# Kernel tuning notes

Measured on AMD Instinct MI355X. Metric: run time of the kernel, lower is better.

The kernel has to match this reference:

```python
import math
import jax, jax.numpy as jnp
import numpy as np

NUM_HEADS = 12


def _key_blocks(x, w):
    # x: [B,S,H,D] -> overlapping key blocks [B, C, 3w, H, D], block c covers
    # original key positions [c*w - w, c*w + 2w) (zero padded at the edges).
    B, S, H, D = x.shape
    C = S // w
    x_pad = jnp.pad(x, ((0, 0), (w, w), (0, 0), (0, 0)))
    idx = (jnp.arange(C) * w)[:, None] + jnp.arange(3 * w)[None, :]  # [C,3w]
    return x_pad[:, idx]


def _band_qk(q, k, w):
    # banded_gemm_qk: scores[b,i,h,j] = q[b,i,h,:] . k[b,i+j-w,h,:], j in [0,2w]
    B, S, H, D = q.shape
    C = S // w
    kb = _key_blocks(k, w)                       # [B,C,3w,H,D]
    qb = q.reshape(B, C, w, H, D)
    s = jnp.einsum('bcxhd,bcyhd->bchxy', qb, kb)  # [B,C,H,w,3w]
    row = jnp.arange(w)[:, None]
    col = row + jnp.arange(2 * w + 1)[None, :]    # diagonal extraction
    band = s[:, :, :, row, col]                   # [B,C,H,w,2w+1]
    return band.transpose(0, 1, 3, 2, 4).reshape(B, S, H, 2 * w + 1)


def _band_pv(p, v, w):
    # banded_gemm_pv: out[b,i,h,:] = sum_j p[b,i,h,j] * v[b,i+j-w,h,:]
    B, S, H, M = p.shape
    C = S // w
    vb = _key_blocks(v, w)                        # [B,C,3w,H,D]
    pb = p.reshape(B, C, w, H, M).transpose(0, 1, 3, 2, 4)  # [B,C,H,w,2w+1]
    row = jnp.arange(w)[:, None]
    col = row + jnp.arange(2 * w + 1)[None, :]
    p_full = jnp.zeros((B, C, H, w, 3 * w), p.dtype).at[:, :, :, row, col].set(pb)
    out = jnp.einsum('bchxy,bcyhd->bcxhd', p_full, vb)  # [B,C,w,H,D]
    return out.reshape(B, S, H, -1)


def setup_inputs():
    key = jax.random.key(0)
    ks = jax.random.split(key, 14)
    B, S, E, G = 2, 4096, 768, 64
    scale = 0.02
    hs = jax.random.normal(ks[0], (B, S, E), jnp.float32)
    mask = jnp.zeros((B, 1, 1, S), jnp.int32).at[:, :, :, :G].set(1)
    def lin(k):
        kw, kb = jax.random.split(k)
        return (jax.random.normal(kw, (E, E), jnp.float32) * scale,
                jax.random.normal(kb, (E,), jnp.float32) * scale)
    Wq, bq = lin(ks[1]); Wk, bk = lin(ks[2]); Wv, bv = lin(ks[3])
    Wqg, bqg = lin(ks[4]); Wkg, bkg = lin(ks[5]); Wvg, bvg = lin(ks[6])
    return dict(hidden_states=hs, attention_mask=mask,
                Wq=Wq, bq=bq, Wk=Wk, bk=bk, Wv=Wv, bv=bv,
                Wqg=Wqg, bqg=bqg, Wkg=Wkg, bkg=bkg, Wvg=Wvg, bvg=bvg,
                window=256, num_global=G)


def reference(hidden_states, attention_mask, Wq, bq, Wk, bk, Wv, bv,
              Wqg, bqg, Wkg, bkg, Wvg, bvg, window, num_global):
    B, S, E = hidden_states.shape
    H = NUM_HEADS
    D = E // H
    w, G = window, num_global
    inv_sqrt_d = 1.0 / math.sqrt(D)

    mask2d = attention_mask.reshape(B, S)
    removed = mask2d != 0  # global (or padding) keys excluded from windowed attn

    q = (hidden_states @ Wq + bq) * inv_sqrt_d
    k = hidden_states @ Wk + bk
    v = hidden_states @ Wv + bv
    q = q.reshape(B, S, H, D)
    k = k.reshape(B, S, H, D)
    v = v.reshape(B, S, H, D)

    # --- local (banded) attention scores ---
    band = _band_qk(q, k, w)                                  # [B,S,H,2w+1]
    key_pos = jnp.arange(S)[:, None] + jnp.arange(-w, w + 1)[None, :]  # [S,2w+1]
    valid = (key_pos >= 0) & (key_pos < S)
    removed_pad = jnp.pad(removed, ((0, 0), (w, w)))
    band_removed = removed_pad[:, key_pos + w]                # [B,S,2w+1]
    keep = valid[None, :, None, :] & (~band_removed)[:, :, None, :]
    band = jnp.where(keep, band, -jnp.inf)

    # --- every-token -> global-token scores (global tokens are first G) ---
    sel = jnp.einsum('blhd,bshd->blhs', q, k[:, :G])          # [B,S,H,G]
    scores = jnp.concatenate([sel, band], axis=-1)            # [B,S,H,G+2w+1]
    probs = jax.nn.softmax(scores.astype(jnp.float32), axis=-1)

    out = jnp.einsum('blhs,bshd->blhd', probs[..., :G], v[:, :G].astype(jnp.float32))
    out = out + _band_pv(probs[..., G:], v.astype(jnp.float32), w)
    out = out.astype(hidden_states.dtype).reshape(B, S, E)

    # --- global tokens attend to everything (separate projections) ---
    hg = hidden_states[:, :G]
    qg = (hg @ Wqg + bqg).reshape(B, G, H, D)
    kg = (hidden_states @ Wkg + bkg).reshape(B, S, H, D)
    vg = (hidden_states @ Wvg + bvg).reshape(B, S, H, D)
    gs = jnp.einsum('bghd,bshd->bhgs', qg, kg) * inv_sqrt_d   # [B,H,G,S]
    gp = jax.nn.softmax(gs.astype(jnp.float32), axis=-1)
    go = jnp.einsum('bhgs,bshd->bghd', gp, vg.astype(jnp.float32)).reshape(B, G, E)
    out = out.at[:, :G].set(go.astype(out.dtype))
    return out
```

## Files before the change

kernel.cpp:

```cpp
#include <hip/hip_runtime.h>
#include <hip/hip_bf16.h>


#define BB 2
#define SS 4096
#define EE 768
#define HH 12
#define DD 64
#define WW 256
#define GG 64
#define NSPLIT 16

typedef unsigned short u16;
typedef __attribute__((ext_vector_type(4))) float f4v;
typedef __attribute__((ext_vector_type(8))) short s8v;
typedef __attribute__((ext_vector_type(4))) short s4v;
typedef __attribute__((ext_vector_type(4))) int i4v;
typedef __attribute__((ext_vector_type(4))) unsigned short us4v;

#define MFMA_BF16(a, b, c) __builtin_amdgcn_mfma_f32_16x16x32_bf16((a), (b), (c), 0, 0, 0)

#if __has_builtin(__builtin_amdgcn_mfma_f32_16x16x16bf16_1k)
#define HAVE_MFMA16 1
#define MFMA16(a, b, c) __builtin_amdgcn_mfma_f32_16x16x16bf16_1k((a), (b), (c), 0, 0, 0)
#else
#define HAVE_MFMA16 0
#endif

constexpr long NSE     = (long)BB * SS * EE;
constexpr long OFF_HSB = 0;
constexpr long OFF_WT  = OFF_HSB + NSE;
constexpr long OFF_Q   = OFF_WT + 6L * EE * EE;
constexpr long OFF_K   = OFF_Q + NSE;
constexpr long OFF_V   = OFF_K + NSE;
constexpr long OFF_KG  = OFF_V + NSE;
constexpr long OFF_VG  = OFF_KG + NSE;
constexpr long OFF_QG  = OFF_VG + NSE;
constexpr long OFF_VT  = OFF_QG + (long)BB * GG * EE;
constexpr long OFF_VGT = OFF_VT + NSE;

constexpr long NQTILE = (long)BB * HH * 4;
constexpr int  NLB    = BB * HH * 63;

__device__ __forceinline__ u16 f2bf(float f) {
  unsigned u = __float_as_uint(f);
  u += 0x7fffu + ((u >> 16) & 1u);
  return (u16)(u >> 16);
}

__device__ __forceinline__ unsigned pk_bf16(float a, float b) {
  union { __hip_bfloat162 h; unsigned u; } c;
  c.h = __float22bfloat162_rn(make_float2(a, b));
  return c.u;
}

__global__ __launch_bounds__(256) void k_prep(const float* __restrict__ hs,
                                              const float* __restrict__ Wq, const float* __restrict__ Wk,
                                              const float* __restrict__ Wv, const float* __restrict__ Wkg,
                                              const float* __restrict__ Wvg, const float* __restrict__ Wqg,
                                              u16* __restrict__ ws) {
  int bid = blockIdx.x;
  if (bid < 6144) {
    long i = ((long)bid * 256 + threadIdx.x) * 4;
    f4v v = *(const f4v*)(hs + i);
    us4v o;
#pragma unroll
    for (int j = 0; j < 4; ++j) o[j] = f2bf(v[j]);
    *(us4v*)(ws + OFF_HSB + i) = o;
    return;
  }
  int wb = bid - 6144;
  int widx = wb / 576; int rem = wb % 576; int kt = rem / 24; int nt = rem % 24;
  const float* src;
  switch (widx) {
    case 0: src = Wq; break; case 1: src = Wk; break; case 2: src = Wv; break;
    case 3: src = Wkg; break; case 4: src = Wvg; break; default: src = Wqg; break;
  }
  __shared__ float tl[32][33];
  int t = threadIdx.x; int r = t >> 3; int c4 = (t & 7) * 4;
  f4v v = *(const f4v*)(src + (long)(kt * 32 + r) * EE + nt * 32 + c4);
#pragma unroll
  for (int j = 0; j < 4; ++j) tl[r][c4 + j] = v[j];
  __syncthreads();
  us4v o;
#pragma unroll
  for (int j = 0; j < 4; ++j) o[j] = f2bf(tl[c4 + j][r]);
  *(us4v*)(ws + OFF_WT + (long)widx * EE * EE + (long)(nt * 32 + r) * EE + kt * 32 + c4) = o;
}

__global__ __launch_bounds__(256, 4) void k_proj(u16* __restrict__ ws,
                                              const float* __restrict__ bq, const float* __restrict__ bk,
                                              const float* __restrict__ bv, const float* __restrict__ bkg,
                                              const float* __restrict__ bvg, const float* __restrict__ bqg) {
  int bid = blockIdx.x;
  int widx, mt, nt;
  if (bid < 1920) {
    int L = (bid & 7) * 240 + (bid >> 3);
    mt = L / 30; int inner = L % 30; widx = inner / 6; nt = inner % 6;
  } else { widx = 5; mt = 0; nt = bid - 1920; }

  __shared__ u16 Al[128 * 64];
  __shared__ u16 Bl[128 * 64];
  int tid = threadIdx.x, lane = tid & 63, wid = tid >> 6;
  int wr = wid >> 1, wc = wid & 1;

  f4v acc[4][4];
#pragma unroll
  for (int i = 0; i < 4; ++i)
#pragma unroll
    for (int j = 0; j < 4; ++j) acc[i][j] = f4v{0.f, 0.f, 0.f, 0.f};

  const u16* hsb = ws + OFF_HSB;
  const u16* Wp  = ws + OFF_WT + (long)widx * EE * EE;

  const u16* asrc[4]; const u16* bsrc[4];
  int dso[4];
#pragma unroll
  for (int it = 0; it < 4; ++it) {
    int c = tid + it * 256;
    int r = c >> 3, j = c & 7;
    long arow;
    if (widx == 5) { int rr = mt * 128 + r; arow = (long)(rr >> 6) * SS + (rr & 63); }
    else           { arow = (long)mt * 128 + r; }
    asrc[it] = hsb + arow * EE + j * 8;
    bsrc[it] = Wp + (long)(nt * 128 + r) * EE + j * 8;
    dso[it]  = r * 64 + (j ^ (r & 7)) * 8;
  }

  const u16* afp[4]; const u16* bfp[4];
#pragma unroll
  for (int f = 0; f < 4; ++f) {
    afp[f] = Al + (wr * 64 + f * 16 + (lane & 15)) * 64;
    bfp[f] = Bl + (wc * 64 + f * 16 + (lane & 15)) * 64;
  }
  int hi4 = lane >> 4, lx = lane & 7;

  i4v areg[4], breg[4];
#pragma unroll
  for (int it = 0; it < 4; ++it) {
    areg[it] = *(const i4v*)(asrc[it]);
    breg[it] = *(const i4v*)(bsrc[it]);
  }
#pragma unroll
  for (int it = 0; it < 4; ++it) {
    *(i4v*)&Al[dso[it]] = areg[it];
    *(i4v*)&Bl[dso[it]] = breg[it];
  }
  __syncthreads();

  for (int t = 0; t < 12; ++t) {
    if (t < 11) {
      int k0n = (t + 1) * 64;
#pragma unroll
      for (int it = 0; it < 4; ++it) {
        areg[it] = *(const i4v*)(asrc[it] + k0n);
        breg[it] = *(const i4v*)(bsrc[it] + k0n);
      }
    }
#pragma unroll
    for (int ks = 0; ks < 2; ++ks) {
      int sw = ((ks * 4 + hi4) ^ lx) * 8;
      s8v af[4], bfr[4];
#pragma unroll
      for (int f = 0; f < 4; ++f) {
        af[f]  = *(const s8v*)(afp[f] + sw);
        bfr[f] = *(const s8v*)(bfp[f] + sw);
      }
#pragma unroll
      for (int i = 0; i < 4; ++i)
#pragma unroll
        for (int j = 0; j < 4; ++j) acc[i][j] = MFMA_BF16(af[i], bfr[j], acc[i][j]);
    }
    __syncthreads();
    if (t < 11) {
#pragma unroll
      for (int it = 0; it < 4; ++it) {
        *(i4v*)&Al[dso[it]] = areg[it];
        *(i4v*)&Bl[dso[it]] = breg[it];
      }
    }
    __syncthreads();
  }

  const float* bias; u16* outp; float scl = 1.0f;
  switch (widx) {
    case 0: bias = bq;  outp = ws + OFF_Q;  scl = 0.125f * 1.44269504f; break;
    case 1: bias = bk;  outp = ws + OFF_K;  break;
    case 2: bias = bv;  outp = ws + OFF_VT;  break;
    case 3: bias = bkg; outp = ws + OFF_KG; break;
    case 4: bias = bvg; outp = ws + OFF_VGT; break;
    default: bias = bqg; outp = ws + OFF_QG; scl = 0.125f * 1.44269504f; break;
  }

  if (widx == 2 || widx == 4) {
    int s0g = mt * 128 + wr * 64 + (lane >> 4) * 4;
#pragma unroll
    for (int fi = 0; fi < 4; ++fi) {
      int srow = s0g + fi * 16;
      int b_ = srow >> 12; int sl = srow & (SS - 1);
#pragma unroll
      for (int fj = 0; fj < 4; ++fj) {
        int col = nt * 128 + wc * 64 + fj * 16 + (lane & 15);
        float bcol = bias[col];
        us4v o;
#pragma unroll
        for (int e = 0; e < 4; ++e) o[e] = f2bf(acc[fi][fj][e] + bcol);
        *(us4v*)&outp[((long)(b_ * HH + (col >> 6)) * DD + (col & 63)) * SS + sl] = o;
      }
    }
  } else {
#pragma unroll
    for (int fi = 0; fi < 4; ++fi)
#pragma unroll
      for (int fj = 0; fj < 4; ++fj) {
        int col = nt * 128 + wc * 64 + fj * 16 + (lane & 15);
        float bcol = bias[col];
#pragma unroll
        for (int e = 0; e < 4; ++e) {
          int rl = wr * 64 + fi * 16 + (lane >> 4) * 4 + e;
          float vv = (acc[fi][fj][e] + bcol) * scl;
          outp[(long)(mt * 128 + rl) * EE + col] = f2bf(vv);
        }
      }
  }
}

__global__ __launch_bounds__(256) void k_lattn(const u16* __restrict__ ws, float* __restrict__ out) {
  int bid0 = blockIdx.x;
  if (bid0 >= NLB) {
    int g = bid0 - NLB;
    int b = g / (HH * 4); int rem = g % (HH * 4); int h = rem >> 2; int qs = rem & 3;
    int tid = threadIdx.x;
    int row = tid >> 4; int c4 = (tid & 15) * 4;

    const float* PA = (const float*)(ws + OFF_V);
    const float* Pm = PA + NQTILE * NSPLIT * 1024L;
    const float* Pl2 = Pm + NQTILE * NSPLIT * 16L;
    long base = (long)g * NSPLIT;

    float M = -1e30f;
#pragma unroll
    for (int s = 0; s < NSPLIT; ++s) M = fmaxf(M, Pm[(base + s) * 16 + row]);
    f4v acc = f4v{0.f, 0.f, 0.f, 0.f};
    float L = 0.f;
#pragma unroll
    for (int s = 0; s < NSPLIT; ++s) {
      float wgt = exp2f(Pm[(base + s) * 16 + row] - M);
      L += wgt * Pl2[(base + s) * 16 + row];
      f4v a = *(const f4v*)&PA[(base + s) * 1024 + row * 64 + c4];
#pragma unroll
      for (int j = 0; j < 4; ++j) acc[j] += wgt * a[j];
    }
    float inv = 1.f / L;
    f4v o;
#pragma unroll
    for (int j = 0; j < 4; ++j) o[j] = acc[j] * inv;
    *(f4v*)&out[((long)b * SS + qs * 16 + row) * EE + h * DD + c4] = o;
    return;
  }

  int bid = (bid0 & 7) * 189 + (bid0 >> 3);
  int b = bid / (HH * 63); int rem = bid % (HH * 63); int h = rem / 63; int qt = rem % 63;
  int l0 = GG + qt * 64;
  int tid = threadIdx.x, lane = tid & 63, wid = tid >> 6;
  int l15 = lane & 15, hi4 = lane >> 4;

  __shared__ u16 Kl[64][72];
  __shared__ u16 Vtl[64][72];
#if !HAVE_MFMA16
  __shared__ u16 Pl[4][16][72];
#endif

  const u16* Qp  = ws + OFF_Q + (long)b * SS * EE;
  const u16* Kp  = ws + OFF_K + (long)b * SS * EE;
  const u16* Vtp = ws + OFF_VT + (long)(b * HH + h) * DD * SS;

  int qbase = l0 + wid * 16;
  s8v qf[2];
#pragma unroll
  for (int ks = 0; ks < 2; ++ks)
    qf[ks] = *(const s8v*)(Qp + (long)(qbase + l15) * EE + h * DD + ks * 32 + hi4 * 8);

  f4v ao[4];
#pragma unroll
  for (int df = 0; df < 4; ++df) ao[df] = f4v{0.f, 0.f, 0.f, 0.f};

  int lo = (l0 - WW > GG) ? (l0 - WW) : GG;
  int hi = (l0 + 64 + WW < SS) ? (l0 + 64 + WW) : SS;
  int ntile = 1 + ((hi - lo) >> 6);

  const u16* kbase[2]; const u16* vbase[2];
  u16* kdst[2]; u16* vdst[2];
#pragma unroll
  for (int it = 0; it < 2; ++it) {
    int c = tid + it * 256;
    int sr = c >> 3, so = (c & 7) * 8;
    kbase[it] = Kp + (long)sr * EE + h * DD + so;
    vbase[it] = Vtp + (long)sr * SS + so;
    kdst[it] = &Kl[sr][so];
    vdst[it] = &Vtl[sr][so];
  }

  i4v kreg[2], vreg[2];
#pragma unroll
  for (int it = 0; it < 2; ++it) {
    kreg[it] = *(const i4v*)(kbase[it]);
    vreg[it] = *(const i4v*)(vbase[it]);
  }
#pragma unroll
  for (int it = 0; it < 2; ++it) {
    *(i4v*)kdst[it] = kreg[it];
    *(i4v*)vdst[it] = vreg[it];
  }
  __syncthreads();

#if HAVE_MFMA16
  float m_s = -1e30f, l_p = 0.f;

  for (int t = 0; t < ntile; ++t) {
    int kb = (t == 0) ? 0 : lo + (t - 1) * 64;
    if (t + 1 < ntile) {
      int kbn = lo + t * 64;
#pragma unroll
      for (int it = 0; it < 2; ++it) {
        kreg[it] = *(const i4v*)(kbase[it] + (long)kbn * EE);
        vreg[it] = *(const i4v*)(vbase[it] + kbn);
      }
    }

    f4v sc[4];
#pragma unroll
    for (int c = 0; c < 4; ++c) sc[c] = f4v{0.f, 0.f, 0.f, 0.f};
    __builtin_amdgcn_s_setprio(1);
#pragma unroll
    for (int c = 0; c < 4; ++c)
#pragma unroll
      for (int ks = 0; ks < 2; ++ks) {
        s8v kf = *(const s8v*)&Kl[c * 16 + l15][ks * 32 + hi4 * 8];
        sc[c] = MFMA_BF16(kf, qf[ks], sc[c]);
      }
    __builtin_amdgcn_s_setprio(0);

    if (t > 0 && (kb <= l0 - WW || kb >= l0 + WW)) {
      int qrow = qbase + l15;
#pragma unroll
      for (int c = 0; c < 4; ++c)
#pragma unroll
        for (int e = 0; e < 4; ++e) {
          int key = kb + c * 16 + hi4 * 4 + e;
          if (key < qrow - WW || key > qrow + WW) sc[c][e] = -1e30f;
        }
    }

    float pmax = sc[0][0];
#pragma unroll
    for (int c = 0; c < 4; ++c)
#pragma unroll
      for (int e = 0; e < 4; ++e) pmax = fmaxf(pmax, sc[c][e]);

    bool need = (t == 0) || !__all(pmax <= m_s + 11.5f);
    if (need) {
      float rm = pmax;
      rm = fmaxf(rm, __shfl_xor(rm, 16));
      rm = fmaxf(rm, __shfl_xor(rm, 32));
      float mn = fmaxf(m_s, rm);
      float scl = exp2f(m_s - mn);
      l_p *= scl;
      float s0 = __shfl(scl, hi4 * 4 + 0);
      float s1 = __shfl(scl, hi4 * 4 + 1);
      float s2 = __shfl(scl, hi4 * 4 + 2);
      float s3 = __shfl(scl, hi4 * 4 + 3);
#pragma unroll
      for (int df = 0; df < 4; ++df) {
        ao[df][0] *= s0; ao[df][1] *= s1; ao[df][2] *= s2; ao[df][3] *= s3;
      }
      m_s = mn;
    }

    unsigned u01[4], u23[4];
#pragma unroll
    for (int c = 0; c < 4; ++c) {
      float p0 = exp2f(sc[c][0] - m_s);
      float p1 = exp2f(sc[c][1] - m_s);
      float p2 = exp2f(sc[c][2] - m_s);
      float p3 = exp2f(sc[c][3] - m_s);
      l_p += (p0 + p1) + (p2 + p3);
      u01[c] = pk_bf16(p0, p1);
      u23[c] = pk_bf16(p2, p3);
    }

    __builtin_amdgcn_s_setprio(1);
#pragma unroll
    for (int c = 0; c < 4; ++c) {
      union { s4v v; unsigned u[2]; } pa;
      pa.u[0] = u01[c]; pa.u[1] = u23[c];
#pragma unroll
      for (int df = 0; df < 4; ++df) {
        s4v vf = *(const s4v*)&Vtl[df * 16 + l15][c * 16 + hi4 * 4];
        ao[df] = MFMA16(pa.v, vf, ao[df]);
      }
    }
    __builtin_amdgcn_s_setprio(0);
    __syncthreads();

    if (t + 1 < ntile) {
#pragma unroll
      for (int it = 0; it < 2; ++it) {
        *(i4v*)kdst[it] = kreg[it];
        *(i4v*)vdst[it] = vreg[it];
      }
    }
    __syncthreads();
  }

  float l_row = l_p;
  l_row += __shfl_xor(l_row, 16);
  l_row += __shfl_xor(l_row, 32);
  float lq[4];
#pragma unroll
  for (int e = 0; e < 4; ++e) lq[e] = __shfl(l_row, hi4 * 4 + e);
#pragma unroll
  for (int df = 0; df < 4; ++df)
#pragma unroll
    for (int e = 0; e < 4; ++e) {
      int row = qbase + hi4 * 4 + e;
      int col = h * DD + df * 16 + l15;
      out[((long)b * SS + row) * EE + col] = ao[df][e] / lq[e];
    }

#else
  float m_r[4], l_p4[4];
#pragma unroll
  for (int e = 0; e < 4; ++e) { m_r[e] = -1e30f; l_p4[e] = 0.f; }

  for (int t = 0; t < ntile; ++t) {
    int kb = (t == 0) ? 0 : lo + (t - 1) * 64;
    if (t + 1 < ntile) {
      int kbn = lo + t * 64;
#pragma unroll
      for (int it = 0; it < 2; ++it) {
        kreg[it] = *(const i4v*)(kbase[it] + (long)kbn * EE);
        vreg[it] = *(const i4v*)(vbase[it] + kbn);
      }
    }

    f4v sc[4];
#pragma unroll
    for (int c = 0; c < 4; ++c) sc[c] = f4v{0.f, 0.f, 0.f, 0.f};
    __builtin_amdgcn_s_setprio(1);
#pragma unroll
    for (int c = 0; c < 4; ++c)
#pragma unroll
      for (int ks = 0; ks < 2; ++ks) {
        s8v kf = *(const s8v*)&Kl[c * 16 + l15][ks * 32 + hi4 * 8];
        sc[c] = MFMA_BF16(qf[ks], kf, sc[c]);
      }
    __builtin_amdgcn_s_setprio(0);

    if (t > 0 && (kb <= l0 - WW || kb >= l0 + WW)) {
#pragma unroll
      for (int c = 0; c < 4; ++c) {
        int key = kb + c * 16 + l15;
#pragma unroll
        for (int e = 0; e < 4; ++e) {
          int qrow = qbase + hi4 * 4 + e;
          if (key < qrow - WW || key > qrow + WW) sc[c][e] = -1e30f;
        }
      }
    }

    float pmax[4];
#pragma unroll
    for (int e = 0; e < 4; ++e)
      pmax[e] = fmaxf(fmaxf(sc[0][e], sc[1][e]), fmaxf(sc[2][e], sc[3][e]));
    bool need;
    if (t == 0) need = true;
    else {
      bool ok = (pmax[0] <= m_r[0] + 11.5f) & (pmax[1] <= m_r[1] + 11.5f) &
                (pmax[2] <= m_r[2] + 11.5f) & (pmax[3] <= m_r[3] + 11.5f);
      need = !__all(ok);
    }
    if (need) {
#pragma unroll
      for (int e = 0; e < 4; ++e) {
        float rm = pmax[e];
#pragma unroll
        for (int off = 1; off < 16; off <<= 1) rm = fmaxf(rm, __shfl_xor(rm, off));
        float mn = fmaxf(m_r[e], rm);
        float scl = exp2f(m_r[e] - mn);
        l_p4[e] *= scl;
#pragma unroll
        for (int df = 0; df < 4; ++df) ao[df][e] *= scl;
        m_r[e] = mn;
      }
    }

#pragma unroll
    for (int e = 0; e < 4; ++e) {
      float p0 = exp2f(sc[0][e] - m_r[e]);
      float p1 = exp2f(sc[1][e] - m_r[e]);
      float p2 = exp2f(sc[2][e] - m_r[e]);
      float p3 = exp2f(sc[3][e] - m_r[e]);
      l_p4[e] += (p0 + p1) + (p2 + p3);
      unsigned u01 = pk_bf16(p0, p1);
      unsigned u23 = pk_bf16(p2, p3);
      int pr = hi4 * 4 + e;
      Pl[wid][pr][l15]      = (u16)u01;
      Pl[wid][pr][16 + l15] = (u16)(u01 >> 16);
      Pl[wid][pr][32 + l15] = (u16)u23;
      Pl[wid][pr][48 + l15] = (u16)(u23 >> 16);
    }

    __builtin_amdgcn_s_setprio(1);
#pragma unroll
    for (int kblk = 0; kblk < 2; ++kblk) {
      s8v pf = *(const s8v*)&Pl[wid][l15][kblk * 32 + hi4 * 8];
#pragma unroll
      for (int df = 0; df < 4; ++df) {
        s8v vf = *(const s8v*)&Vtl[df * 16 + l15][kblk * 32 + hi4 * 8];
        ao[df] = MFMA_BF16(pf, vf, ao[df]);
      }
    }
    __builtin_amdgcn_s_setprio(0);
    __syncthreads();

    if (t + 1 < ntile) {
#pragma unroll
      for (int it = 0; it < 2; ++it) {
        *(i4v*)kdst[it] = kreg[it];
        *(i4v*)vdst[it] = vreg[it];
      }
    }
    __syncthreads();
  }

  float l_r[4];
#pragma unroll
  for (int e = 0; e < 4; ++e) {
    float s = l_p4[e];
#pragma unroll
    for (int off = 1; off < 16; off <<= 1) s += __shfl_xor(s, off);
    l_r[e] = s;
  }
#pragma unroll
  for (int df = 0; df < 4; ++df)
#pragma unroll
    for (int e = 0; e < 4; ++e) {
      int row = qbase + hi4 * 4 + e;
      int col = h * DD + df * 16 + l15;
      out[((long)b * SS + row) * EE + col] = ao[df][e] / l_r[e];
    }
#endif
}

__global__ __launch_bounds__(64) void k_gattn_part(u16* __restrict__ ws) {
  int bid = blockIdx.x;
  int g = bid / NSPLIT; int sp = bid % NSPLIT;
  int b = g / (HH * 4); int rem = g % (HH * 4); int h = rem >> 2; int qs = rem & 3;
  int lane = threadIdx.x;

  __shared__ u16 Kl[32][72];
  __shared__ u16 Vtl[64][40];
  __shared__ u16 Pl[16][40];

  const u16* Qgp = ws + OFF_QG + (long)b * GG * EE;
  const u16* Kgp = ws + OFF_KG + (long)b * SS * EE;
  const u16* Vtp = ws + OFF_VGT + (long)(b * HH + h) * DD * SS;

  int qbase = qs * 16;
  s8v qf[2];
#pragma unroll
  for (int ks = 0; ks < 2; ++ks)
    qf[ks] = *(const s8v*)(Qgp + (long)(qbase + (lane & 15)) * EE + h * DD + ks * 32 + (lane >> 4) * 8);

  float m_r[4], l_p[4]; f4v ao[4];
#pragma unroll
  for (int e = 0; e < 4; ++e) { m_r[e] = -1e30f; l_p[e] = 0.f; }
#pragma unroll
  for (int df = 0; df < 4; ++df) ao[df] = f4v{0.f, 0.f, 0.f, 0.f};

  int t0 = sp * (SS / 32 / NSPLIT);
  for (int kt = t0; kt < t0 + SS / 32 / NSPLIT; ++kt) {
    int kb = kt * 32;
#pragma unroll
    for (int r2 = 0; r2 < 4; ++r2) {
      int chunk = lane + r2 * 64;
      int kr = chunk >> 3, ko = (chunk & 7) * 8;
      *(i4v*)&Kl[kr][ko] = *(const i4v*)(Kgp + (long)(kb + kr) * EE + h * DD + ko);
      int dr = chunk >> 2, ko2 = (chunk & 3) * 8;
      *(i4v*)&Vtl[dr][ko2] = *(const i4v*)(Vtp + (long)dr * SS + kb + ko2);
    }
    __syncthreads();

    f4v sc[2] = {f4v{0.f, 0.f, 0.f, 0.f}, f4v{0.f, 0.f, 0.f, 0.f}};
#pragma unroll
    for (int c = 0; c < 2; ++c)
#pragma unroll
      for (int ks = 0; ks < 2; ++ks) {
        s8v kf = *(const s8v*)&Kl[c * 16 + (lane & 15)][ks * 32 + (lane >> 4) * 8];
        sc[c] = MFMA_BF16(qf[ks], kf, sc[c]);
      }

    float pmax[4];
#pragma unroll
    for (int e = 0; e < 4; ++e) pmax[e] = fmaxf(sc[0][e], sc[1][e]);
    bool need;
    if (kt == t0) need = true;
    else {
      bool ok = (pmax[0] <= m_r[0] + 11.5f) & (pmax[1] <= m_r[1] + 11.5f) &
                (pmax[2] <= m_r[2] + 11.5f) & (pmax[3] <= m_r[3] + 11.5f);
      need = !__all(ok);
    }
    if (need) {
#pragma unroll
      for (int e = 0; e < 4; ++e) {
        float rm = pmax[e];
#pragma unroll
        for (int off = 1; off < 16; off <<= 1) rm = fmaxf(rm, __shfl_xor(rm, off));
        float mn = fmaxf(m_r[e], rm);
        float scl = exp2f(m_r[e] - mn);
        l_p[e] *= scl;
#pragma unroll
        for (int df = 0; df < 4; ++df) ao[df][e] *= scl;
        m_r[e] = mn;
      }
    }

#pragma unroll
    for (int e = 0; e < 4; ++e) {
      float p0 = exp2f(sc[0][e] - m_r[e]);
      float p1 = exp2f(sc[1][e] - m_r[e]);
      l_p[e] += p0 + p1;
      unsigned u01 = pk_bf16(p0, p1);
      int pr = (lane >> 4) * 4 + e;
      int l15 = lane & 15;
      Pl[pr][l15]      = (u16)u01;
      Pl[pr][16 + l15] = (u16)(u01 >> 16);
    }
    s8v pf = *(const s8v*)&Pl[lane & 15][(lane >> 4) * 8];
#pragma unroll
    for (int df = 0; df < 4; ++df) {
      s8v vf = *(const s8v*)&Vtl[df * 16 + (lane & 15)][(lane >> 4) * 8];
      ao[df] = MFMA_BF16(pf, vf, ao[df]);
    }
    __syncthreads();
  }

  float l_r[4];
#pragma unroll
  for (int e = 0; e < 4; ++e) {
    float s = l_p[e];
#pragma unroll
    for (int off = 1; off < 16; off <<= 1) s += __shfl_xor(s, off);
    l_r[e] = s;
  }

  float* PA = (float*)(ws + OFF_V);
  float* Pm = PA + NQTILE * NSPLIT * 1024L;
  float* Pl2 = Pm + NQTILE * NSPLIT * 16L;
  long pb = (long)g * NSPLIT + sp;
#pragma unroll
  for (int df = 0; df < 4; ++df)
#pragma unroll
    for (int e = 0; e < 4; ++e) {
      int rl = (lane >> 4) * 4 + e;
      PA[pb * 1024 + rl * 64 + df * 16 + (lane & 15)] = ao[df][e];
    }
  if ((lane & 15) == 0) {
#pragma unroll
    for (int e = 0; e < 4; ++e) {
      int rl = (lane >> 4) * 4 + e;
      Pm[pb * 16 + rl] = m_r[e];
      Pl2[pb * 16 + rl] = l_r[e];
    }
  }
}

extern "C" void kernel_launch(void* const* d_in, const int* in_sizes, int n_in,
                              void* d_out, int out_size, void* d_ws, size_t ws_size,
                              hipStream_t stream) {
  const float* hs  = (const float*)d_in[0];
  const float* Wq  = (const float*)d_in[2];  const float* bq  = (const float*)d_in[3];
  const float* Wk  = (const float*)d_in[4];  const float* bk  = (const float*)d_in[5];
  const float* Wv  = (const float*)d_in[6];  const float* bv  = (const float*)d_in[7];
  const float* Wqg = (const float*)d_in[8];  const float* bqg = (const float*)d_in[9];
  const float* Wkg = (const float*)d_in[10]; const float* bkg = (const float*)d_in[11];
  const float* Wvg = (const float*)d_in[12]; const float* bvg = (const float*)d_in[13];
  u16* ws = (u16*)d_ws;
  float* out = (float*)d_out;

  k_prep<<<6144 + 6 * 24 * 24, 256, 0, stream>>>(hs, Wq, Wk, Wv, Wkg, Wvg, Wqg, ws);
  k_proj<<<1926, 256, 0, stream>>>(ws, bq, bk, bv, bkg, bvg, bqg);
  k_gattn_part<<<(int)(NQTILE * NSPLIT), 64, 0, stream>>>(ws);
  k_lattn<<<NLB + (int)NQTILE, 256, 0, stream>>>(ws, out);
}
```

Baseline: 134.1 us.

## Deepen projection GEMM prefetch and double-buffer attention K/V tiles

```diff
diff --git a/kernel.cpp b/kernel.cpp
--- a/kernel.cpp
+++ b/kernel.cpp
@@ -135,28 +135,19 @@
   }
   int hi4 = lane >> 4, lx = lane & 7;
 
-  i4v areg[4], breg[4];
-#pragma unroll
-  for (int it = 0; it < 4; ++it) {
-    areg[it] = *(const i4v*)(asrc[it]);
-    breg[it] = *(const i4v*)(bsrc[it]);
-  }
-#pragma unroll
-  for (int it = 0; it < 4; ++it) {
-    *(i4v*)&Al[dso[it]] = areg[it];
-    *(i4v*)&Bl[dso[it]] = breg[it];
-  }
+  i4v a0[4], b0[4], a1[4], b1[4];
+#pragma unroll
+  for (int it = 0; it < 4; ++it) { a0[it] = *(const i4v*)(asrc[it]); b0[it] = *(const i4v*)(bsrc[it]); }
+#pragma unroll
+  for (int it = 0; it < 4; ++it) { *(i4v*)&Al[dso[it]] = a0[it]; *(i4v*)&Bl[dso[it]] = b0[it]; }
+#pragma unroll
+  for (int it = 0; it < 4; ++it) { a0[it] = *(const i4v*)(asrc[it] + 64);  b0[it] = *(const i4v*)(bsrc[it] + 64); }
+#pragma unroll
+  for (int it = 0; it < 4; ++it) { a1[it] = *(const i4v*)(asrc[it] + 128); b1[it] = *(const i4v*)(bsrc[it] + 128); }
   __syncthreads();
 
+#pragma unroll
   for (int t = 0; t < 12; ++t) {
-    if (t < 11) {
-      int k0n = (t + 1) * 64;
-#pragma unroll
-      for (int it = 0; it < 4; ++it) {
-        areg[it] = *(const i4v*)(asrc[it] + k0n);
-        breg[it] = *(const i4v*)(bsrc[it] + k0n);
-      }
-    }
 #pragma unroll
     for (int ks = 0; ks < 2; ++ks) {
       int sw = ((ks * 4 + hi4) ^ lx) * 8;
@@ -173,10 +164,22 @@
     }
     __syncthreads();
     if (t < 11) {
-#pragma unroll
-      for (int it = 0; it < 4; ++it) {
-        *(i4v*)&Al[dso[it]] = areg[it];
-        *(i4v*)&Bl[dso[it]] = breg[it];
+      if ((t & 1) == 0) {
+#pragma unroll
+        for (int it = 0; it < 4; ++it) { *(i4v*)&Al[dso[it]] = a0[it]; *(i4v*)&Bl[dso[it]] = b0[it]; }
+        if (t < 9) {
+          int k0n = (t + 3) * 64;
+#pragma unroll
+          for (int it = 0; it < 4; ++it) { a0[it] = *(const i4v*)(asrc[it] + k0n); b0[it] = *(const i4v*)(bsrc[it] + k0n); }
+        }
+      } else {
+#pragma unroll
+        for (int it = 0; it < 4; ++it) { *(i4v*)&Al[dso[it]] = a1[it]; *(i4v*)&Bl[dso[it]] = b1[it]; }
+        if (t < 9) {
+          int k0n = (t + 3) * 64;
+#pragma unroll
+          for (int it = 0; it < 4; ++it) { a1[it] = *(const i4v*)(asrc[it] + k0n); b1[it] = *(const i4v*)(bsrc[it] + k0n); }
+        }
       }
     }
     __syncthreads();
@@ -265,8 +268,8 @@
   int tid = threadIdx.x, lane = tid & 63, wid = tid >> 6;
   int l15 = lane & 15, hi4 = lane >> 4;
 
-  __shared__ u16 Kl[64][72];
-  __shared__ u16 Vtl[64][72];
+  __shared__ u16 Kl[2][64][72];
+  __shared__ u16 Vtl[2][64][72];
 #if !HAVE_MFMA16
   __shared__ u16 Pl[4][16][72];
 #endif
@@ -290,15 +293,18 @@
   int ntile = 1 + ((hi - lo) >> 6);
 
   const u16* kbase[2]; const u16* vbase[2];
-  u16* kdst[2]; u16* vdst[2];
+  u16* kdstb[2][2]; u16* vdstb[2][2];
 #pragma unroll
   for (int it = 0; it < 2; ++it) {
     int c = tid + it * 256;
     int sr = c >> 3, so = (c & 7) * 8;
     kbase[it] = Kp + (long)sr * EE + h * DD + so;
     vbase[it] = Vtp + (long)sr * SS + so;
-    kdst[it] = &Kl[sr][so];
-    vdst[it] = &Vtl[sr][so];
+#pragma unroll
+    for (int bf = 0; bf < 2; ++bf) {
+      kdstb[bf][it] = &Kl[bf][sr][so];
+      vdstb[bf][it] = &Vtl[bf][sr][so];
+    }
   }
 
   i4v kreg[2], vreg[2];
@@ -309,8 +315,8 @@
   }
 #pragma unroll
   for (int it = 0; it < 2; ++it) {
-    *(i4v*)kdst[it] = kreg[it];
-    *(i4v*)vdst[it] = vreg[it];
+    *(i4v*)kdstb[0][it] = kreg[it];
+    *(i4v*)vdstb[0][it] = vreg[it];
   }
   __syncthreads();
 
@@ -318,6 +324,7 @@
   float m_s = -1e30f, l_p = 0.f;
 
   for (int t = 0; t < ntile; ++t) {
+    int cur = t & 1;
     int kb = (t == 0) ? 0 : lo + (t - 1) * 64;
     if (t + 1 < ntile) {
       int kbn = lo + t * 64;
@@ -336,7 +343,7 @@
     for (int c = 0; c < 4; ++c)
 #pragma unroll
       for (int ks = 0; ks < 2; ++ks) {
-        s8v kf = *(const s8v*)&Kl[c * 16 + l15][ks * 32 + hi4 * 8];
+        s8v kf = *(const s8v*)&Kl[cur][c * 16 + l15][ks * 32 + hi4 * 8];
         sc[c] = MFMA_BF16(kf, qf[ks], sc[c]);
       }
     __builtin_amdgcn_s_setprio(0);
@@ -396,18 +403,17 @@
       pa.u[0] = u01[c]; pa.u[1] = u23[c];
 #pragma unroll
       for (int df = 0; df < 4; ++df) {
-        s4v vf = *(const s4v*)&Vtl[df * 16 + l15][c * 16 + hi4 * 4];
+        s4v vf = *(const s4v*)&Vtl[cur][df * 16 + l15][c * 16 + hi4 * 4];
         ao[df] = MFMA16(pa.v, vf, ao[df]);
       }
     }
     __builtin_amdgcn_s_setprio(0);
-    __syncthreads();
 
     if (t + 1 < ntile) {
 #pragma unroll
       for (int it = 0; it < 2; ++it) {
-        *(i4v*)kdst[it] = kreg[it];
-        *(i4v*)vdst[it] = vreg[it];
+        *(i4v*)kdstb[cur ^ 1][it] = kreg[it];
+        *(i4v*)vdstb[cur ^ 1][it] = vreg[it];
       }
     }
     __syncthreads();
@@ -434,6 +440,7 @@
   for (int e = 0; e < 4; ++e) { m_r[e] = -1e30f; l_p4[e] = 0.f; }
 
   for (int t = 0; t < ntile; ++t) {
+    int cur = t & 1;
     int kb = (t == 0) ? 0 : lo + (t - 1) * 64;
     if (t + 1 < ntile) {
       int kbn = lo + t * 64;
@@ -452,7 +459,7 @@
     for (int c = 0; c < 4; ++c)
 #pragma unroll
       for (int ks = 0; ks < 2; ++ks) {
-        s8v kf = *(const s8v*)&Kl[c * 16 + l15][ks * 32 + hi4 * 8];
+        s8v kf = *(const s8v*)&Kl[cur][c * 16 + l15][ks * 32 + hi4 * 8];
         sc[c] = MFMA_BF16(qf[ks], kf, sc[c]);
       }
     __builtin_amdgcn_s_setprio(0);
@@ -517,18 +524,17 @@
       s8v pf = *(const s8v*)&Pl[wid][l15][kblk * 32 + hi4 * 8];
 #pragma unroll
       for (int df = 0; df < 4; ++df) {
-        s8v vf = *(const s8v*)&Vtl[df * 16 + l15][kblk * 32 + hi4 * 8];
+        s8v vf = *(const s8v*)&Vtl[cur][df * 16 + l15][kblk * 32 + hi4 * 8];
         ao[df] = MFMA_BF16(pf, vf, ao[df]);
       }
     }
     __builtin_amdgcn_s_setprio(0);
-    __syncthreads();
 
     if (t + 1 < ntile) {
 #pragma unroll
       for (int it = 0; it < 2; ++it) {
-        *(i4v*)kdst[it] = kreg[it];
-        *(i4v*)vdst[it] = vreg[it];
+        *(i4v*)kdstb[cur ^ 1][it] = kreg[it];
+        *(i4v*)vdstb[cur ^ 1][it] = vreg[it];
       }
     }
     __syncthreads();
```

Result: slower. 287.8 us (+114.6%).

## Fuse global-attention partials into local-attention launch, split combine into own kernel

Applied to the files above, without the earlier changes.

```diff
diff --git a/kernel.cpp b/kernel.cpp
--- a/kernel.cpp
+++ b/kernel.cpp
@@ -41,6 +41,7 @@
 
 constexpr long NQTILE = (long)BB * HH * 4;
 constexpr int  NLB    = BB * HH * 63;
+constexpr int  NPB    = (int)(NQTILE * NSPLIT / 4);
 
 __device__ __forceinline__ u16 f2bf(float f) {
   unsigned u = __float_as_uint(f);
@@ -225,50 +226,143 @@
   }
 }
 
-__global__ __launch_bounds__(256) void k_lattn(const u16* __restrict__ ws, float* __restrict__ out) {
+__global__ __launch_bounds__(256) void k_fused(const u16* __restrict__ ws, float* __restrict__ out) {
+  int tid = threadIdx.x, lane = tid & 63, wid = tid >> 6;
+  int l15 = lane & 15, hi4 = lane >> 4;
+  __shared__ __align__(16) char smem[44032];
   int bid0 = blockIdx.x;
+
   if (bid0 >= NLB) {
-    int g = bid0 - NLB;
+    int task = (bid0 - NLB) * 4 + wid;
+    int g = task >> 4; int sp = task & 15;
     int b = g / (HH * 4); int rem = g % (HH * 4); int h = rem >> 2; int qs = rem & 3;
-    int tid = threadIdx.x;
-    int row = tid >> 4; int c4 = (tid & 15) * 4;
-
-    const float* PA = (const float*)(ws + OFF_V);
-    const float* Pm = PA + NQTILE * NSPLIT * 1024L;
-    const float* Pl2 = Pm + NQTILE * NSPLIT * 16L;
-    long base = (long)g * NSPLIT;
-
-    float M = -1e30f;
-#pragma unroll
-    for (int s = 0; s < NSPLIT; ++s) M = fmaxf(M, Pm[(base + s) * 16 + row]);
-    f4v acc = f4v{0.f, 0.f, 0.f, 0.f};
-    float L = 0.f;
-#pragma unroll
-    for (int s = 0; s < NSPLIT; ++s) {
-      float wgt = exp2f(Pm[(base + s) * 16 + row] - M);
-      L += wgt * Pl2[(base + s) * 16 + row];
-      f4v a = *(const f4v*)&PA[(base + s) * 1024 + row * 64 + c4];
-#pragma unroll
-      for (int j = 0; j < 4; ++j) acc[j] += wgt * a[j];
-    }
-    float inv = 1.f / L;
-    f4v o;
-#pragma unroll
-    for (int j = 0; j < 4; ++j) o[j] = acc[j] * inv;
-    *(f4v*)&out[((long)b * SS + qs * 16 + row) * EE + h * DD + c4] = o;
+
+    char* base = smem + wid * 11008;
+    u16 (*Kl2)[72] = (u16(*)[72])base;
+    u16 (*Vt2)[40] = (u16(*)[40])(base + 4608);
+    u16 (*Pw)[40]  = (u16(*)[40])(base + 9728);
+
+    const u16* Qgp = ws + OFF_QG + (long)b * GG * EE;
+    const u16* Kgp = ws + OFF_KG + (long)b * SS * EE;
+    const u16* Vtp = ws + OFF_VGT + (long)(b * HH + h) * DD * SS;
+
+    int qbase = qs * 16;
+    s8v qf[2];
+#pragma unroll
+    for (int ks = 0; ks < 2; ++ks)
+      qf[ks] = *(const s8v*)(Qgp + (long)(qbase + l15) * EE + h * DD + ks * 32 + hi4 * 8);
+
+    float m_r[4], l_p[4]; f4v ao[4];
+#pragma unroll
+    for (int e = 0; e < 4; ++e) { m_r[e] = -1e30f; l_p[e] = 0.f; }
+#pragma unroll
+    for (int df = 0; df < 4; ++df) ao[df] = f4v{0.f, 0.f, 0.f, 0.f};
+
+    int t0 = sp * (SS / 32 / NSPLIT);
+    for (int kt = t0; kt < t0 + SS / 32 / NSPLIT; ++kt) {
+      int kb = kt * 32;
+#pragma unroll
+      for (int r2 = 0; r2 < 4; ++r2) {
+        int chunk = lane + r2 * 64;
+        int kr = chunk >> 3, ko = (chunk & 7) * 8;
+        *(i4v*)&Kl2[kr][ko] = *(const i4v*)(Kgp + (long)(kb + kr) * EE + h * DD + ko);
+        int dr = chunk >> 2, ko2 = (chunk & 3) * 8;
+        *(i4v*)&Vt2[dr][ko2] = *(const i4v*)(Vtp + (long)dr * SS + kb + ko2);
+      }
+      __syncthreads();
+
+      f4v sc[2] = {f4v{0.f, 0.f, 0.f, 0.f}, f4v{0.f, 0.f, 0.f, 0.f}};
+#pragma unroll
+      for (int c = 0; c < 2; ++c)
+#pragma unroll
+        for (int ks = 0; ks < 2; ++ks) {
+          s8v kf = *(const s8v*)&Kl2[c * 16 + l15][ks * 32 + hi4 * 8];
+          sc[c] = MFMA_BF16(qf[ks], kf, sc[c]);
+        }
+
+      float pmax[4];
+#pragma unroll
+      for (int e = 0; e < 4; ++e) pmax[e] = fmaxf(sc[0][e], sc[1][e]);
+      bool need;
+      if (kt == t0) need = true;
+      else {
+        bool ok = (pmax[0] <= m_r[0] + 11.5f) & (pmax[1] <= m_r[1] + 11.5f) &
+                  (pmax[2] <= m_r[2] + 11.5f) & (pmax[3] <= m_r[3] + 11.5f);
+        need = !__all(ok);
+      }
+      if (need) {
+#pragma unroll
+        for (int e = 0; e < 4; ++e) {
+          float rm = pmax[e];
+#pragma unroll
+          for (int off = 1; off < 16; off <<= 1) rm = fmaxf(rm, __shfl_xor(rm, off));
+          float mn = fmaxf(m_r[e], rm);
+          float scl = exp2f(m_r[e] - mn);
+          l_p[e] *= scl;
+#pragma unroll
+          for (int df = 0; df < 4; ++df) ao[df][e] *= scl;
+          m_r[e] = mn;
+        }
+      }
+
+#pragma unroll
+      for (int e = 0; e < 4; ++e) {
+        float p0 = exp2f(sc[0][e] - m_r[e]);
+        float p1 = exp2f(sc[1][e] - m_r[e]);
+        l_p[e] += p0 + p1;
+        unsigned u01 = pk_bf16(p0, p1);
+        int pr = hi4 * 4 + e;
+        Pw[pr][l15]      = (u16)u01;
+        Pw[pr][16 + l15] = (u16)(u01 >> 16);
+      }
+      s8v pf = *(const s8v*)&Pw[l15][hi4 * 8];
+#pragma unroll
+      for (int df = 0; df < 4; ++df) {
+        s8v vf = *(const s8v*)&Vt2[df * 16 + l15][hi4 * 8];
+        ao[df] = MFMA_BF16(pf, vf, ao[df]);
+      }
+      __syncthreads();
+    }
+
+    float l_r[4];
+#pragma unroll
+    for (int e = 0; e < 4; ++e) {
+      float s = l_p[e];
+#pragma unroll
+      for (int off = 1; off < 16; off <<= 1) s += __shfl_xor(s, off);
+      l_r[e] = s;
+    }
+
+    float* PA = (float*)(ws + OFF_V);
+    float* Pm = PA + NQTILE * NSPLIT * 1024L;
+    float* Pl2 = Pm + NQTILE * NSPLIT * 16L;
+    long pb = (long)g * NSPLIT + sp;
+#pragma unroll
+    for (int df = 0; df < 4; ++df)
+#pragma unroll
+      for (int e = 0; e < 4; ++e) {
+        int rl = hi4 * 4 + e;
+        PA[pb * 1024 + rl * 64 + df * 16 + l15] = ao[df][e];
+      }
+    if (l15 == 0) {
+#pragma unroll
+      for (int e = 0; e < 4; ++e) {
+        int rl = hi4 * 4 + e;
+        Pm[pb * 16 + rl] = m_r[e];
+        Pl2[pb * 16 + rl] = l_r[e];
+      }
+    }
     return;
   }
 
   int bid = (bid0 & 7) * 189 + (bid0 >> 3);
   int b = bid / (HH * 63); int rem = bid % (HH * 63); int h = rem / 63; int qt = rem % 63;
   int l0 = GG + qt * 64;
-  int tid = threadIdx.x, lane = tid & 63, wid = tid >> 6;
-  int l15 = lane & 15, hi4 = lane >> 4;
-
-  __shared__ u16 Kl[64][72];
-  __shared__ u16 Vtl[64][72];
+
+  u16 (*Kl)[72]  = (u16(*)[72])smem;
+  u16 (*Vtl)[72] = (u16(*)[72])(smem + 9216);
 #if !HAVE_MFMA16
-  __shared__ u16 Pl[4][16][72];
+  u16 (*Pl)[16][72] = (u16(*)[16][72])(smem + 18432);
 #endif
 
   const u16* Qp  = ws + OFF_Q + (long)b * SS * EE;
@@ -553,127 +647,35 @@
 #endif
 }
 
-__global__ __launch_bounds__(64) void k_gattn_part(u16* __restrict__ ws) {
-  int bid = blockIdx.x;
-  int g = bid / NSPLIT; int sp = bid % NSPLIT;
+__global__ __launch_bounds__(256) void k_gcomb(const u16* __restrict__ ws, float* __restrict__ out) {
+  int g = blockIdx.x;
   int b = g / (HH * 4); int rem = g % (HH * 4); int h = rem >> 2; int qs = rem & 3;
-  int lane = threadIdx.x;
-
-  __shared__ u16 Kl[32][72];
-  __shared__ u16 Vtl[64][40];
-  __shared__ u16 Pl[16][40];
-
-  const u16* Qgp = ws + OFF_QG + (long)b * GG * EE;
-  const u16* Kgp = ws + OFF_KG + (long)b * SS * EE;
-  const u16* Vtp = ws + OFF_VGT + (long)(b * HH + h) * DD * SS;
-
-  int qbase = qs * 16;
-  s8v qf[2];
-#pragma unroll
-  for (int ks = 0; ks < 2; ++ks)
-    qf[ks] = *(const s8v*)(Qgp + (long)(qbase + (lane & 15)) * EE + h * DD + ks * 32 + (lane >> 4) * 8);
-
-  float m_r[4], l_p[4]; f4v ao[4];
-#pragma unroll
-  for (int e = 0; e < 4; ++e) { m_r[e] = -1e30f; l_p[e] = 0.f; }
-#pragma unroll
-  for (int df = 0; df < 4; ++df) ao[df] = f4v{0.f, 0.f, 0.f, 0.f};
-
-  int t0 = sp * (SS / 32 / NSPLIT);
-  for (int kt = t0; kt < t0 + SS / 32 / NSPLIT; ++kt) {
-    int kb = kt * 32;
-#pragma unroll
-    for (int r2 = 0; r2 < 4; ++r2) {
-      int chunk = lane + r2 * 64;
-      int kr = chunk >> 3, ko = (chunk & 7) * 8;
-      *(i4v*)&Kl[kr][ko] = *(const i4v*)(Kgp + (long)(kb + kr) * EE + h * DD + ko);
-      int dr = chunk >> 2, ko2 = (chunk & 3) * 8;
-      *(i4v*)&Vtl[dr][ko2] = *(const i4v*)(Vtp + (long)dr * SS + kb + ko2);
-    }
-    __syncthreads();
-
-    f4v sc[2] = {f4v{0.f, 0.f, 0.f, 0.f}, f4v{0.f, 0.f, 0.f, 0.f}};
-#pragma unroll
-    for (int c = 0; c < 2; ++c)
-#pragma unroll
-      for (int ks = 0; ks < 2; ++ks) {
-        s8v kf = *(const s8v*)&Kl[c * 16 + (lane & 15)][ks * 32 + (lane >> 4) * 8];
-        sc[c] = MFMA_BF16(qf[ks], kf, sc[c]);
-      }
-
-    float pmax[4];
-#pragma unroll
-    for (int e = 0; e < 4; ++e) pmax[e] = fmaxf(sc[0][e], sc[1][e]);
-    bool need;
-    if (kt == t0) need = true;
-    else {
-      bool ok = (pmax[0] <= m_r[0] + 11.5f) & (pmax[1] <= m_r[1] + 11.5f) &
-                (pmax[2] <= m_r[2] + 11.5f) & (pmax[3] <= m_r[3] + 11.5f);
-      need = !__all(ok);
-    }
-    if (need) {
-#pragma unroll
-      for (int e = 0; e < 4; ++e) {
-        float rm = pmax[e];
-#pragma unroll
-        for (int off = 1; off < 16; off <<= 1) rm = fmaxf(rm, __shfl_xor(rm, off));
-        float mn = fmaxf(m_r[e], rm);
-        float scl = exp2f(m_r[e] - mn);
-        l_p[e] *= scl;
-#pragma unroll
-        for (int df = 0; df < 4; ++df) ao[df][e] *= scl;
-        m_r[e] = mn;
-      }
-    }
-
-#pragma unroll
-    for (int e = 0; e < 4; ++e) {
-      float p0 = exp2f(sc[0][e] - m_r[e]);
-      float p1 = exp2f(sc[1][e] - m_r[e]);
-      l_p[e] += p0 + p1;
-      unsigned u01 = pk_bf16(p0, p1);
-      int pr = (lane >> 4) * 4 + e;
-      int l15 = lane & 15;
-      Pl[pr][l15]      = (u16)u01;
-      Pl[pr][16 + l15] = (u16)(u01 >> 16);
-    }
-    s8v pf = *(const s8v*)&Pl[lane & 15][(lane >> 4) * 8];
-#pragma unroll
-    for (int df = 0; df < 4; ++df) {
-      s8v vf = *(const s8v*)&Vtl[df * 16 + (lane & 15)][(lane >> 4) * 8];
-      ao[df] = MFMA_BF16(pf, vf, ao[df]);
-    }
-    __syncthreads();
-  }
-
-  float l_r[4];
-#pragma unroll
-  for (int e = 0; e < 4; ++e) {
-    float s = l_p[e];
-#pragma unroll
-    for (int off = 1; off < 16; off <<= 1) s += __shfl_xor(s, off);
-    l_r[e] = s;
-  }
-
-  float* PA = (float*)(ws + OFF_V);
-  float* Pm = PA + NQTILE * NSPLIT * 1024L;
-  float* Pl2 = Pm + NQTILE * NSPLIT * 16L;
-  long pb = (long)g * NSPLIT + sp;
-#pragma unroll
-  for (int df = 0; df < 4; ++df)
-#pragma unroll
-    for (int e = 0; e < 4; ++e) {
-      int rl = (lane >> 4) * 4 + e;
-      PA[pb * 1024 + rl * 64 + df * 16 + (lane & 15)] = ao[df][e];
-    }
-  if ((lane & 15) == 0) {
-#pragma unroll
-    for (int e = 0; e < 4; ++e) {
-      int rl = (lane >> 4) * 4 + e;
-      Pm[pb * 16 + rl] = m_r[e];
-      Pl2[pb * 16 + rl] = l_r[e];
-    }
-  }
+  int tid = threadIdx.x;
+  int row = tid >> 4; int c4 = (tid & 15) * 4;
+
+  const float* PA = (const float*)(ws + OFF_V);
+  const float* Pm = PA + NQTILE * NSPLIT * 1024L;
+  const float* Pl2 = Pm + NQTILE * NSPLIT * 16L;
+  long base = (long)g * NSPLIT;
+
+  float M = -1e30f;
+#pragma unroll
+  for (int s = 0; s < NSPLIT; ++s) M = fmaxf(M, Pm[(base + s) * 16 + row]);
+  f4v acc = f4v{0.f, 0.f, 0.f, 0.f};
+  float L = 0.f;
+#pragma unroll
+  for (int s = 0; s < NSPLIT; ++s) {
+    float wgt = exp2f(Pm[(base + s) * 16 + row] - M);
+    L += wgt * Pl2[(base + s) * 16 + row];
+    f4v a = *(const f4v*)&PA[(base + s) * 1024 + row * 64 + c4];
+#pragma unroll
+    for (int j = 0; j < 4; ++j) acc[j] += wgt * a[j];
+  }
+  float inv = 1.f / L;
+  f4v o;
+#pragma unroll
+  for (int j = 0; j < 4; ++j) o[j] = acc[j] * inv;
+  *(f4v*)&out[((long)b * SS + qs * 16 + row) * EE + h * DD + c4] = o;
 }
 
 extern "C" void kernel_launch(void* const* d_in, const int* in_sizes, int n_in,
@@ -691,6 +693,6 @@
 
   k_prep<<<6144 + 6 * 24 * 24, 256, 0, stream>>>(hs, Wq, Wk, Wv, Wkg, Wvg, Wqg, ws);
   k_proj<<<1926, 256, 0, stream>>>(ws, bq, bk, bv, bkg, bvg, bqg);
-  k_gattn_part<<<(int)(NQTILE * NSPLIT), 64, 0, stream>>>(ws);
-  k_lattn<<<NLB + (int)NQTILE, 256, 0, stream>>>(ws, out);
+  k_fused<<<NLB + NPB, 256, 0, stream>>>(ws, out);
+  k_gcomb<<<(int)NQTILE, 256, 0, stream>>>(ws, out);
 }
```

Result: no change. 132.5 us (-1.2%).
